# Optimization experiments

Hardware: AMD Instinct MI355X
Metric: run time of the kernel (lower is better)

## Reference

```python
import jax, jax.numpy as jnp
from jax import lax
import numpy as np

NUM_LABELS = 64
ENC_DIM = 256
C = 128            # channels
C2 = 2 * C         # trunk width
OUT_DIM = 512
LAYERS = [(3, 1), (3, 2), (3, 4), (3, 8), (3, 16)]
RF = 1 + sum((k - 1) * d for k, d in LAYERS)   # 63
MAX_T = 48
PAD, START, STOP = 0, 5, 6
BATCH, T_ENC = 8, 64


def setup_inputs() -> dict:
    key = jax.random.key(0)
    ks = jax.random.split(key, 20)

    def w(k, shape, fan_in):
        return (jax.random.normal(k, shape, jnp.float32) * np.sqrt(2.0 / fan_in)).astype(jnp.float32)

    def b(k, shape):
        return 1e-4 * jax.random.normal(k, shape, jnp.float32)

    L = len(LAYERS)
    return {
        'encoded_seq': jax.random.normal(ks[0], (BATCH, ENC_DIM, T_ENC), jnp.float32),
        'embed':  w(ks[1], (NUM_LABELS, C2), NUM_LABELS),
        'w_in':   w(ks[2], (C2, C2), C2),      'b_in':  b(ks[3], (C2,)),
        'w_enc':  w(ks[4], (ENC_DIM, C2), ENC_DIM), 'b_enc': b(ks[5], (C2,)),
        'res_w1': w(ks[6], (L, C2, C), C2),    'res_b1': b(ks[7], (L, C)),
        'res_wd': w(ks[8], (L, 3, C, C), 3 * C), 'res_bd': b(ks[9], (L, C)),
        'res_w2': w(ks[10], (L, C, C2), C),    'res_b2': b(ks[11], (L, C2)),
        'w_o1':   w(ks[12], (C2, OUT_DIM), C2), 'b_o1': b(ks[13], (OUT_DIM,)),
        'w_o2':   w(ks[14], (OUT_DIM, NUM_LABELS), OUT_DIM), 'b_o2': b(ks[15], (NUM_LABELS,)),
    }


def _decode(encoded_seq, embed, w_in, b_in, w_enc, b_enc,
            res_w1, res_b1, res_wd, res_bd, res_w2, res_b2,
            w_o1, b_o1, w_o2, b_o2):
    B = encoded_seq.shape[0]
    # left-pad encoding with rf-1 zeros (torch code leaves these uninitialized; zeros used here)
    encoded_pad = jnp.concatenate(
        [jnp.zeros((B, ENC_DIM, RF - 1), encoded_seq.dtype), encoded_seq], axis=2)

    def linear(labels, enc_win):
        # labels: (B, RF) int32; enc_win: (B, ENC_DIM, RF)
        x = embed[labels]                                     # (B, RF, C2)
        x = x @ w_in + b_in                                   # input 1x1 conv
        x = x + jnp.einsum('bct,cd->btd', enc_win, w_enc) + b_enc
        for i, (kk, d) in enumerate(LAYERS):                  # ReLU residual blocks
            h = jax.nn.relu(x)
            h = jax.nn.relu(h @ res_w1[i] + res_b1[i])        # 2c -> c
            h = lax.conv_general_dilated(                     # causal dilated conv c -> c
                h, res_wd[i], window_strides=(1,), padding=[((kk - 1) * d, 0)],
                rhs_dilation=(d,), dimension_numbers=('NWC', 'WIO', 'NWC')) + res_bd[i]
            h = jax.nn.relu(h)
            x = x + (h @ res_w2[i] + res_b2[i])               # c -> 2c, residual
        o = jax.nn.relu(x @ w_o1 + b_o1) @ w_o2 + b_o2        # (B, RF, NUM_LABELS)
        return o[:, -1, :]                                    # last timestep only

    def step(labels, k):
        enc_win = lax.dynamic_slice(encoded_pad, (0, 0, k), (B, ENC_DIM, RF))
        logit = linear(labels, enc_win)                       # (B, NUM_LABELS)
        nxt = jnp.argmax(logit, axis=-1).astype(jnp.int32)
        labels = jnp.concatenate([labels[:, 1:], nxt[:, None]], axis=1)
        return labels, (logit, nxt)

    init_labels = jnp.concatenate(
        [jnp.full((B, RF - 1), PAD, jnp.int32), jnp.full((B, 1), START, jnp.int32)], axis=1)
    _, (logits, nexts) = lax.scan(step, init_labels, jnp.arange(MAX_T))
    logits = jnp.transpose(logits, (1, 2, 0))                 # (B, NUM_LABELS, T)
    stopped = jnp.cumsum((nexts == STOP).astype(jnp.int32), axis=0) >= 1  # (T, B), incl. current step
    lengths = (MAX_T - stopped.sum(axis=0)).astype(jnp.int32)
    return logits, lengths


def reference(encoded_seq, embed, w_in, b_in, w_enc, b_enc,
              res_w1, res_b1, res_wd, res_bd, res_w2, res_b2,
              w_o1, b_o1, w_o2, b_o2):
    return _decode(encoded_seq, embed, w_in, b_in, w_enc, b_enc,
                   res_w1, res_b1, res_wd, res_bd, res_w2, res_b2,
                   w_o1, b_o1, w_o2, b_o2)
```

## Files before the change

### kernel.cpp

```cpp
#include <hip/hip_runtime.h>
#include <hip/hip_bf16.h>

#define NUM_LABELS 64
#define ENC_DIM 256
#define CC 128
#define C2 256
#define OUT_DIM 512
#define NLAYERS 5
#define MAX_T 48
#define BATCH 8
#define T_ENC 64
#define LAB_PAD 0
#define LAB_START 5
#define LAB_STOP 6

__device__ __forceinline__ float dot4(float4 wv, float4 av) {
    return wv.x * av.x + wv.y * av.y + wv.z * av.z + wv.w * av.w;
}

__global__ __launch_bounds__(256) void pre_kernel(
    const float* __restrict__ enc, const float* __restrict__ embed,
    const float* __restrict__ w_in, const float* __restrict__ b_in,
    const float* __restrict__ w_enc, const float* __restrict__ b_enc,
    float* __restrict__ E2, float* __restrict__ encp)
{
    const int t = threadIdx.x;
    const int blk = blockIdx.x;
    if (blk < NUM_LABELS) {
        float acc = b_in[t];
        const float* e = embed + blk * C2;
        for (int j = 0; j < C2; ++j) acc += e[j] * w_in[j * C2 + t];
        E2[blk * C2 + t] = acc;
    } else {
        const int idx = blk - NUM_LABELS;
        const int b = idx / MAX_T;
        const int k = idx % MAX_T;
        float acc = b_enc[t];
        const float* ecol = enc + b * ENC_DIM * T_ENC + k;
        for (int c = 0; c < ENC_DIM; ++c) acc += ecol[c * T_ENC] * w_enc[c * C2 + t];
        encp[idx * C2 + t] = acc;
    }
}

__global__ __launch_bounds__(256) void prefix_kernel(
    const float* __restrict__ embed, const float* __restrict__ w_in,
    const float* __restrict__ b_in,  const float* __restrict__ b_enc,
    const float* __restrict__ w1,    const float* __restrict__ b1,
    const float* __restrict__ wd,    const float* __restrict__ bd,
    const float* __restrict__ w2,    const float* __restrict__ b2,
    float* __restrict__ h0out)
{
    const int t = threadIdx.x;
    __shared__ float x[C2];
    __shared__ float r[C2];
    __shared__ float h[CC];
    __shared__ float hr[CC];

    {
        float acc = b_in[t] + b_enc[t];
        const float* e = embed + LAB_PAD * C2;
        for (int j = 0; j < C2; ++j) acc += e[j] * w_in[j * C2 + t];
        x[t] = acc;
    }
    __syncthreads();

    for (int i = 0; i < NLAYERS; ++i) {
        r[t] = fmaxf(x[t], 0.f);
        __syncthreads();
        if (t < CC) {
            float a = b1[i * CC + t];
            const float* W = w1 + (i * C2) * CC + t;
            for (int j = 0; j < C2; ++j) a += r[j] * W[j * CC];
            float hv = fmaxf(a, 0.f);
            h[t] = hv;
            h0out[i * CC + t] = hv;
        }
        __syncthreads();
        if (t < CC) {
            float a = bd[i * CC + t];
            const float* W0 = wd + ((i * 3 + 0) * CC) * CC + t;
            const float* W1 = wd + ((i * 3 + 1) * CC) * CC + t;
            const float* W2 = wd + ((i * 3 + 2) * CC) * CC + t;
            for (int c = 0; c < CC; ++c)
                a += h[c] * (W0[c * CC] + W1[c * CC] + W2[c * CC]);
            hr[t] = fmaxf(a, 0.f);
        }
        __syncthreads();
        {
            float a = b2[i * C2 + t];
            const float* W = w2 + (i * CC) * C2 + t;
            for (int c = 0; c < CC; ++c) a += hr[c] * W[c * C2];
            x[t] += a;
        }
        __syncthreads();
    }
}

__global__ __launch_bounds__(256) void repack_w1_kernel(
    const float* __restrict__ src, float4* __restrict__ dst)
{
    const int p = blockIdx.x * 256 + threadIdx.x;
    const int i = p >> 13, q = p & 8191;
    const int m = q >> 10, t = q & 1023;
    const int g = t >> 7, c = t & 127;
    const int r0 = g * 32 + m * 4;
    const float* s = src + (i * 256 + r0) * 128 + c;
    float4 v; v.x = s[0]; v.y = s[128]; v.z = s[256]; v.w = s[384];
    dst[p] = v;
}

__global__ __launch_bounds__(256) void repack_wd_kernel(
    const float* __restrict__ src, float4* __restrict__ dst)
{
    const int p = blockIdx.x * 256 + threadIdx.x;
    const int i = p / 12288, q = p % 12288;
    const int u = q >> 10, t = q & 1023;
    const int tap = u % 3, m = u / 3;
    const int g = t >> 7, c = t & 127;
    const int r0 = g * 16 + m * 4;
    const float* s = src + ((i * 3 + tap) * 128 + r0) * 128 + c;
    float4 v; v.x = s[0]; v.y = s[128]; v.z = s[256]; v.w = s[384];
    dst[p] = v;
}

__global__ __launch_bounds__(256) void repack_w2_kernel(
    const float* __restrict__ src, float4* __restrict__ dst)
{
    const int p = blockIdx.x * 256 + threadIdx.x;
    const int i = p >> 13, q = p & 8191;
    const int m = q >> 10, t = q & 1023;
    const int g = t >> 8, c = t & 255;
    const int r0 = g * 32 + m * 4;
    const float* s = src + (i * 128 + r0) * 256 + c;
    float4 v; v.x = s[0]; v.y = s[256]; v.z = s[512]; v.w = s[768];
    dst[p] = v;
}

__global__ __launch_bounds__(256) void repack_wo1_kernel(
    const float* __restrict__ src, float4* __restrict__ dst)
{
    const int p = blockIdx.x * 256 + threadIdx.x;
    const int m = p >> 10, t = p & 1023;
    const int g = t >> 9, c = t & 511;
    const int r0 = g * 128 + m * 4;
    const float* s = src + r0 * 512 + c;
    float4 v; v.x = s[0]; v.y = s[512]; v.z = s[1024]; v.w = s[1536];
    dst[p] = v;
}

__global__ __launch_bounds__(256) void repack_wo2_kernel(
    const float* __restrict__ src, float4* __restrict__ dst)
{
    const int p = blockIdx.x * 256 + threadIdx.x;
    const int m = p >> 10, t = p & 1023;
    const int g = t >> 6, c = t & 63;
    const int r0 = g * 32 + m * 4;
    const float* s = src + r0 * 64 + c;
    float4 v; v.x = s[0]; v.y = s[64]; v.z = s[128]; v.w = s[192];
    dst[p] = v;
}

__global__ __launch_bounds__(1024) void decode_kernel(
    const float4* __restrict__ w1L,  const float* __restrict__ b1,
    const float4* __restrict__ wdL,  const float* __restrict__ bd,
    const float4* __restrict__ w2L,  const float* __restrict__ b2,
    const float4* __restrict__ wo1L, const float* __restrict__ bo1,
    const float4* __restrict__ wo2L, const float* __restrict__ bo2,
    const float* __restrict__ E2, const float* __restrict__ encp,
    const float* __restrict__ h0g, float* __restrict__ out)
{
    const int b = blockIdx.x;
    const int t = threadIdx.x;

    __shared__ alignas(16) float ring0[3 * CC];
    __shared__ alignas(16) float ring1[5 * CC];
    __shared__ alignas(16) float ring2[9 * CC];
    __shared__ alignas(16) float ring3[17 * CC];
    __shared__ alignas(16) float ring4[33 * CC];
    __shared__ alignas(16) float h0s[NLAYERS * CC];
    __shared__ alignas(16) float xs[C2];
    __shared__ alignas(16) float rs[C2];
    __shared__ alignas(16) float hr[CC];
    __shared__ alignas(16) float us[OUT_DIM];
    __shared__ alignas(16) float part[1024];
    __shared__ float b1s[NLAYERS * CC];
    __shared__ float bds[NLAYERS * CC];
    __shared__ float b2s[NLAYERS * C2];
    __shared__ float bo1s[OUT_DIM];
    __shared__ float bo2s[NUM_LABELS];
    __shared__ int s_lab, s_stop;

    float* rings[NLAYERS] = { ring0, ring1, ring2, ring3, ring4 };
    const int rszc[NLAYERS] = { 3, 5, 9, 17, 33 };

    for (int idx = t; idx < NLAYERS * CC; idx += 1024) {
        h0s[idx] = h0g[idx]; b1s[idx] = b1[idx]; bds[idx] = bd[idx];
    }
    for (int idx = t; idx < NLAYERS * C2; idx += 1024) b2s[idx] = b2[idx];
    for (int idx = t; idx < OUT_DIM; idx += 1024) bo1s[idx] = bo1[idx];
    for (int idx = t; idx < NUM_LABELS; idx += 1024) bo2s[idx] = bo2[idx];
    if (t == 0) { s_lab = LAB_START; s_stop = MAX_T; }
    __syncthreads();

    for (int k = 0; k < MAX_T; ++k) {
        if (t < C2) {
            float xv = E2[s_lab * C2 + t] + encp[(b * MAX_T + k) * C2 + t];
            xs[t] = xv;
            rs[t] = fmaxf(xv, 0.f);
        }
        __syncthreads();

#pragma unroll
        for (int i = 0; i < NLAYERS; ++i) {
            const int d = 1 << i;
            const int rsz = rszc[i];
            const int cslot = k % rsz;
            float* rng = rings[i];

            {
                const int g = t >> 7;
                const float4* Wb = w1L + i * 8192 + t;
                const float4* ra = reinterpret_cast<const float4*>(rs) + g * 8;
                float4 wv[8], av[8];
#pragma unroll
                for (int m = 0; m < 8; ++m) wv[m] = Wb[m * 1024];
#pragma unroll
                for (int m = 0; m < 8; ++m) av[m] = ra[m];
                float acc = 0.f;
#pragma unroll
                for (int m = 0; m < 8; ++m) acc += dot4(wv[m], av[m]);
                part[t] = acc;
            }
            __syncthreads();
            if (t < CC) {
                float s = b1s[i * CC + t];
#pragma unroll
                for (int g2 = 0; g2 < 8; ++g2) s += part[g2 * 128 + t];
                rng[cslot * CC + t] = fmaxf(s, 0.f);
            }
            __syncthreads();

            {
                const int g = t >> 7;
                const float* cur = rng + cslot * CC;
                const float* p1 = (k >= d)     ? rng + ((k - d) % rsz) * CC     : h0s + i * CC;
                const float* p0 = (k >= 2 * d) ? rng + ((k - 2 * d) % rsz) * CC : h0s + i * CC;
                const float4* c4  = reinterpret_cast<const float4*>(cur) + g * 4;
                const float4* a14 = reinterpret_cast<const float4*>(p1) + g * 4;
                const float4* a04 = reinterpret_cast<const float4*>(p0) + g * 4;
                const float4* Wb = wdL + i * 12288 + t;
                float4 wv[12], av[12];
#pragma unroll
                for (int m = 0; m < 4; ++m) {
                    wv[m * 3 + 0] = Wb[(m * 3 + 0) * 1024];
                    wv[m * 3 + 1] = Wb[(m * 3 + 1) * 1024];
                    wv[m * 3 + 2] = Wb[(m * 3 + 2) * 1024];
                }
#pragma unroll
                for (int m = 0; m < 4; ++m) {
                    av[m * 3 + 0] = a04[m];
                    av[m * 3 + 1] = a14[m];
                    av[m * 3 + 2] = c4[m];
                }
                float acc = 0.f;
#pragma unroll
                for (int m = 0; m < 12; ++m) acc += dot4(wv[m], av[m]);
                part[t] = acc;
            }
            __syncthreads();
            if (t < CC) {
                float s = bds[i * CC + t];
#pragma unroll
                for (int g2 = 0; g2 < 8; ++g2) s += part[g2 * 128 + t];
                hr[t] = fmaxf(s, 0.f);
            }
            __syncthreads();

            {
                const int g = t >> 8;
                const float4* Wb = w2L + i * 8192 + t;
                const float4* ha = reinterpret_cast<const float4*>(hr) + g * 8;
                float4 wv[8], av[8];
#pragma unroll
                for (int m = 0; m < 8; ++m) wv[m] = Wb[m * 1024];
#pragma unroll
                for (int m = 0; m < 8; ++m) av[m] = ha[m];
                float acc = 0.f;
#pragma unroll
                for (int m = 0; m < 8; ++m) acc += dot4(wv[m], av[m]);
                part[t] = acc;
            }
            __syncthreads();
            if (t < C2) {
                float s = b2s[i * C2 + t];
#pragma unroll
                for (int g2 = 0; g2 < 4; ++g2) s += part[g2 * 256 + t];
                float xv = xs[t] + s;
                xs[t] = xv;
                rs[t] = fmaxf(xv, 0.f);
            }
            __syncthreads();
        }

        {
            const int g = t >> 9;
            const float4* Wb = wo1L + t;
            const float4* xa = reinterpret_cast<const float4*>(xs) + g * 32;
            float acc = 0.f;
#pragma unroll 1
            for (int mb = 0; mb < 4; ++mb) {
                float4 wv[8], av[8];
#pragma unroll
                for (int m = 0; m < 8; ++m) wv[m] = Wb[(mb * 8 + m) * 1024];
#pragma unroll
                for (int m = 0; m < 8; ++m) av[m] = xa[mb * 8 + m];
#pragma unroll
                for (int m = 0; m < 8; ++m) acc += dot4(wv[m], av[m]);
            }
            part[t] = acc;
        }
        __syncthreads();
        if (t < OUT_DIM) us[t] = fmaxf(part[t] + part[t + 512] + bo1s[t], 0.f);
        __syncthreads();

        {
            const int g = t >> 6;
            const float4* Wb = wo2L + t;
            const float4* ua = reinterpret_cast<const float4*>(us) + g * 8;
            float4 wv[8], av[8];
#pragma unroll
            for (int m = 0; m < 8; ++m) wv[m] = Wb[m * 1024];
#pragma unroll
            for (int m = 0; m < 8; ++m) av[m] = ua[m];
            float acc = 0.f;
#pragma unroll
            for (int m = 0; m < 8; ++m) acc += dot4(wv[m], av[m]);
            part[t] = acc;
        }
        __syncthreads();
        if (t < NUM_LABELS) {
            float v = bo2s[t];
#pragma unroll
            for (int g2 = 0; g2 < 16; ++g2) v += part[g2 * 64 + t];
            out[(b * NUM_LABELS + t) * MAX_T + k] = v;
            float bv = v; int bi = t;
#pragma unroll
            for (int off = 32; off; off >>= 1) {
                float ov = __shfl_xor(bv, off);
                int oi = __shfl_xor(bi, off);
                if (ov > bv || (ov == bv && oi < bi)) { bv = ov; bi = oi; }
            }
            if (t == 0) {
                s_lab = bi;
                if (bi == LAB_STOP && s_stop == MAX_T) s_stop = k;
            }
        }
        __syncthreads();
    }

    if (t == 0) out[BATCH * NUM_LABELS * MAX_T + b] = (float)s_stop;
}

extern "C" void kernel_launch(void* const* d_in, const int* in_sizes, int n_in,
                              void* d_out, int out_size, void* d_ws, size_t ws_size,
                              hipStream_t stream) {
    const float* enc   = (const float*)d_in[0];
    const float* embed = (const float*)d_in[1];
    const float* w_in  = (const float*)d_in[2];
    const float* b_in  = (const float*)d_in[3];
    const float* w_enc = (const float*)d_in[4];
    const float* b_enc = (const float*)d_in[5];
    const float* w1    = (const float*)d_in[6];
    const float* b1    = (const float*)d_in[7];
    const float* wd    = (const float*)d_in[8];
    const float* bd    = (const float*)d_in[9];
    const float* w2    = (const float*)d_in[10];
    const float* b2    = (const float*)d_in[11];
    const float* wo1   = (const float*)d_in[12];
    const float* bo1   = (const float*)d_in[13];
    const float* wo2   = (const float*)d_in[14];
    const float* bo2   = (const float*)d_in[15];
    float* out = (float*)d_out;
    float* wsf = (float*)d_ws;

    float* E2   = wsf;
    float* encp = wsf + 16384;
    float* h0   = wsf + 16384 + 98304;
    float4* w1L  = (float4*)(wsf + 115328);
    float4* wdL  = w1L + 40960;
    float4* w2L  = wdL + 61440;
    float4* wo1L = w2L + 40960;
    float4* wo2L = wo1L + 32768;

    pre_kernel<<<NUM_LABELS + BATCH * MAX_T, 256, 0, stream>>>(
        enc, embed, w_in, b_in, w_enc, b_enc, E2, encp);
    prefix_kernel<<<1, 256, 0, stream>>>(
        embed, w_in, b_in, b_enc, w1, b1, wd, bd, w2, b2, h0);
    repack_w1_kernel<<<160, 256, 0, stream>>>(w1, w1L);
    repack_wd_kernel<<<240, 256, 0, stream>>>(wd, wdL);
    repack_w2_kernel<<<160, 256, 0, stream>>>(w2, w2L);
    repack_wo1_kernel<<<128, 256, 0, stream>>>(wo1, wo1L);
    repack_wo2_kernel<<<32, 256, 0, stream>>>(wo2, wo2L);
    decode_kernel<<<BATCH, 1024, 0, stream>>>(
        w1L, b1, wdL, bd, w2L, b2, wo1L, bo1, wo2L, bo2, E2, encp, h0, out);
}
```

Baseline: 3.406 ms.

## Split decode across 8 workgroups per batch with global-atomic inter-block sync

Each batch's sequential decode was handled by a single 1024-thread workgroup that streamed all weights from global or L2 memory every step. It now runs on 8 cooperating 256-thread workgroups per batch, 64 in total. Each workgroup owns an output slice, keeps its weight slice in registers, and prefetches the next layer's weights while waiting. Partial activations are exchanged through global memory using agent-scope atomics and counter-based spin barriers. This adds cross-CU synchronisation latency at every matvec stage in exchange for more parallel compute and less weight traffic per workgroup, and it relies on all 64 blocks being co-resident.

```diff
diff --git a/kernel.cpp b/kernel.cpp
--- a/kernel.cpp
+++ b/kernel.cpp
@@ -14,8 +14,22 @@
 #define LAB_START 5
 #define LAB_STOP 6
 
+#define AGENT __HIP_MEMORY_SCOPE_AGENT
+
 __device__ __forceinline__ float dot4(float4 wv, float4 av) {
     return wv.x * av.x + wv.y * av.y + wv.z * av.z + wv.w * av.w;
+}
+
+__device__ __forceinline__ void sync_signal(int* ctr, int t) {
+    __builtin_amdgcn_fence(__ATOMIC_RELEASE, "agent");
+    if (t == 0) __hip_atomic_fetch_add(ctr, 1, __ATOMIC_RELAXED, AGENT);
+}
+__device__ __forceinline__ void sync_wait(int* ctr, int t, int target) {
+    if (t == 0) {
+        while (__hip_atomic_load(ctr, __ATOMIC_RELAXED, AGENT) < target) {}
+    }
+    __builtin_amdgcn_fence(__ATOMIC_ACQUIRE, "agent");
+    __syncthreads();
 }
 
 __global__ __launch_bounds__(256) void pre_kernel(
@@ -100,77 +114,88 @@
     const float* __restrict__ src, float4* __restrict__ dst)
 {
     const int p = blockIdx.x * 256 + threadIdx.x;
-    const int i = p >> 13, q = p & 8191;
-    const int m = q >> 10, t = q & 1023;
-    const int g = t >> 7, c = t & 127;
-    const int r0 = g * 32 + m * 4;
-    const float* s = src + (i * 256 + r0) * 128 + c;
-    float4 v; v.x = s[0]; v.y = s[128]; v.z = s[256]; v.w = s[384];
-    dst[p] = v;
+    const int si = p >> 10, c = p & 1023;
+    const int s = si / 5, i = si % 5;
+    const int m = c >> 8, tt = c & 255;
+    const int g = tt >> 4, o = tt & 15;
+    const float* b = src + (i * 256 + g * 16 + m * 4) * 128 + s * 16 + o;
+    float4 v; v.x = b[0]; v.y = b[128]; v.z = b[256]; v.w = b[384];
+    dst[s * 23040 + i * 3584 + c] = v;
 }
 
 __global__ __launch_bounds__(256) void repack_wd_kernel(
     const float* __restrict__ src, float4* __restrict__ dst)
 {
     const int p = blockIdx.x * 256 + threadIdx.x;
-    const int i = p / 12288, q = p % 12288;
-    const int u = q >> 10, t = q & 1023;
-    const int tap = u % 3, m = u / 3;
-    const int g = t >> 7, c = t & 127;
-    const int r0 = g * 16 + m * 4;
-    const float* s = src + ((i * 3 + tap) * 128 + r0) * 128 + c;
-    float4 v; v.x = s[0]; v.y = s[128]; v.z = s[256]; v.w = s[384];
-    dst[p] = v;
+    const int si = p / 1536, c = p % 1536;
+    const int s = si / 5, i = si % 5;
+    const int u = c >> 8, tt = c & 255;
+    const int tap = u >> 1, m = u & 1;
+    const int g = tt >> 4, o = tt & 15;
+    const float* b = src + ((i * 3 + tap) * 128 + g * 8 + m * 4) * 128 + s * 16 + o;
+    float4 v; v.x = b[0]; v.y = b[128]; v.z = b[256]; v.w = b[384];
+    dst[s * 23040 + i * 3584 + 1024 + c] = v;
 }
 
 __global__ __launch_bounds__(256) void repack_w2_kernel(
     const float* __restrict__ src, float4* __restrict__ dst)
 {
     const int p = blockIdx.x * 256 + threadIdx.x;
-    const int i = p >> 13, q = p & 8191;
-    const int m = q >> 10, t = q & 1023;
-    const int g = t >> 8, c = t & 255;
-    const int r0 = g * 32 + m * 4;
-    const float* s = src + (i * 128 + r0) * 256 + c;
-    float4 v; v.x = s[0]; v.y = s[256]; v.z = s[512]; v.w = s[768];
-    dst[p] = v;
+    const int si = p >> 10, c = p & 1023;
+    const int s = si / 5, i = si % 5;
+    const int m = c >> 8, tt = c & 255;
+    const int g = tt >> 5, o = tt & 31;
+    const float* b = src + (i * 128 + g * 16 + m * 4) * 256 + s * 32 + o;
+    float4 v; v.x = b[0]; v.y = b[256]; v.z = b[512]; v.w = b[768];
+    dst[s * 23040 + i * 3584 + 2560 + c] = v;
 }
 
 __global__ __launch_bounds__(256) void repack_wo1_kernel(
     const float* __restrict__ src, float4* __restrict__ dst)
 {
     const int p = blockIdx.x * 256 + threadIdx.x;
-    const int m = p >> 10, t = p & 1023;
-    const int g = t >> 9, c = t & 511;
-    const int r0 = g * 128 + m * 4;
-    const float* s = src + r0 * 512 + c;
-    float4 v; v.x = s[0]; v.y = s[512]; v.z = s[1024]; v.w = s[1536];
-    dst[p] = v;
+    const int s = p >> 12, c = p & 4095;
+    const int m = c >> 8, tt = c & 255;
+    const int g = tt >> 6, o = tt & 63;
+    const float* b = src + (g * 64 + m * 4) * 512 + s * 64 + o;
+    float4 v; v.x = b[0]; v.y = b[512]; v.z = b[1024]; v.w = b[1536];
+    dst[s * 23040 + 17920 + c] = v;
 }
 
 __global__ __launch_bounds__(256) void repack_wo2_kernel(
     const float* __restrict__ src, float4* __restrict__ dst)
 {
     const int p = blockIdx.x * 256 + threadIdx.x;
-    const int m = p >> 10, t = p & 1023;
-    const int g = t >> 6, c = t & 63;
-    const int r0 = g * 32 + m * 4;
-    const float* s = src + r0 * 64 + c;
-    float4 v; v.x = s[0]; v.y = s[64]; v.z = s[128]; v.w = s[192];
-    dst[p] = v;
-}
-
-__global__ __launch_bounds__(1024) void decode_kernel(
-    const float4* __restrict__ w1L,  const float* __restrict__ b1,
-    const float4* __restrict__ wdL,  const float* __restrict__ bd,
-    const float4* __restrict__ w2L,  const float* __restrict__ b2,
-    const float4* __restrict__ wo1L, const float* __restrict__ bo1,
-    const float4* __restrict__ wo2L, const float* __restrict__ bo2,
+    const int s = p >> 10, c = p & 1023;
+    const int m = c >> 8, tt = c & 255;
+    const int g = tt >> 3, o = tt & 7;
+    const float* b = src + (g * 16 + m * 4) * 64 + s * 8 + o;
+    float4 v; v.x = b[0]; v.y = b[64]; v.z = b[128]; v.w = b[192];
+    dst[s * 23040 + 22016 + c] = v;
+}
+
+__global__ __launch_bounds__(256) void init_ctr_kernel(int* __restrict__ ctrs)
+{
+    const int idx = blockIdx.x * 256 + threadIdx.x;
+    if (idx < 512) ctrs[idx] = 0;
+}
+
+__global__ __launch_bounds__(256) void decode_kernel(
+    const float4* __restrict__ Wall,
+    const float* __restrict__ b1, const float* __restrict__ bd,
+    const float* __restrict__ b2, const float* __restrict__ bo1,
+    const float* __restrict__ bo2,
     const float* __restrict__ E2, const float* __restrict__ encp,
-    const float* __restrict__ h0g, float* __restrict__ out)
-{
-    const int b = blockIdx.x;
+    const float* __restrict__ h0g,
+    float* __restrict__ actH, float* __restrict__ actHR,
+    float* __restrict__ actX, float* __restrict__ actU,
+    float* __restrict__ actLG, int* __restrict__ ctrs,
+    float* __restrict__ out)
+{
+    const int e = blockIdx.x & 7;
+    const int s = blockIdx.x >> 3;
     const int t = threadIdx.x;
+    const float4* W4 = Wall + s * 23040;
 
     __shared__ alignas(16) float ring0[3 * CC];
     __shared__ alignas(16) float ring1[5 * CC];
@@ -180,31 +205,30 @@
     __shared__ alignas(16) float h0s[NLAYERS * CC];
     __shared__ alignas(16) float xs[C2];
     __shared__ alignas(16) float rs[C2];
-    __shared__ alignas(16) float hr[CC];
+    __shared__ alignas(16) float hfull[CC];
+    __shared__ alignas(16) float hrf[CC];
     __shared__ alignas(16) float us[OUT_DIM];
-    __shared__ alignas(16) float part[1024];
-    __shared__ float b1s[NLAYERS * CC];
-    __shared__ float bds[NLAYERS * CC];
-    __shared__ float b2s[NLAYERS * C2];
-    __shared__ float bo1s[OUT_DIM];
-    __shared__ float bo2s[NUM_LABELS];
+    __shared__ float part[256];
     __shared__ int s_lab, s_stop;
 
-    float* rings[NLAYERS] = { ring0, ring1, ring2, ring3, ring4 };
-    const int rszc[NLAYERS] = { 3, 5, 9, 17, 33 };
-
-    for (int idx = t; idx < NLAYERS * CC; idx += 1024) {
-        h0s[idx] = h0g[idx]; b1s[idx] = b1[idx]; bds[idx] = bd[idx];
-    }
-    for (int idx = t; idx < NLAYERS * C2; idx += 1024) b2s[idx] = b2[idx];
-    for (int idx = t; idx < OUT_DIM; idx += 1024) bo1s[idx] = bo1[idx];
-    for (int idx = t; idx < NUM_LABELS; idx += 1024) bo2s[idx] = bo2[idx];
+    for (int i = t; i < NLAYERS * CC; i += 256) h0s[i] = h0g[i];
     if (t == 0) { s_lab = LAB_START; s_stop = MAX_T; }
     __syncthreads();
 
+    int* ctr = ctrs + e * 64;
+    int target = 8;
+
+    float4 wA[4], wB[6], wC[4], wD[16], wE[4];
+
+    {
+        const float4* p = W4;
+#pragma unroll
+        for (int m = 0; m < 4; ++m) wA[m] = p[m * 256 + t];
+    }
+
     for (int k = 0; k < MAX_T; ++k) {
-        if (t < C2) {
-            float xv = E2[s_lab * C2 + t] + encp[(b * MAX_T + k) * C2 + t];
+        {
+            float xv = E2[s_lab * C2 + t] + encp[(e * MAX_T + k) * C2 + t];
             xs[t] = xv;
             rs[t] = fmaxf(xv, 0.f);
         }
@@ -213,89 +237,108 @@
 #pragma unroll
         for (int i = 0; i < NLAYERS; ++i) {
             const int d = 1 << i;
-            const int rsz = rszc[i];
-            const int cslot = k % rsz;
-            float* rng = rings[i];
-
-            {
-                const int g = t >> 7;
-                const float4* Wb = w1L + i * 8192 + t;
-                const float4* ra = reinterpret_cast<const float4*>(rs) + g * 8;
-                float4 wv[8], av[8];
-#pragma unroll
-                for (int m = 0; m < 8; ++m) wv[m] = Wb[m * 1024];
-#pragma unroll
-                for (int m = 0; m < 8; ++m) av[m] = ra[m];
+            const int rsz = (2 * d + 1);
+            float* rng = (i == 0) ? ring0 : (i == 1) ? ring1 : (i == 2) ? ring2
+                        : (i == 3) ? ring3 : ring4;
+
+            {
+                const int g = t >> 4;
+                const float4* rs4 = (const float4*)rs;
                 float acc = 0.f;
 #pragma unroll
-                for (int m = 0; m < 8; ++m) acc += dot4(wv[m], av[m]);
+                for (int m = 0; m < 4; ++m) acc += dot4(wA[m], rs4[g * 4 + m]);
                 part[t] = acc;
             }
             __syncthreads();
+            if (t < 16) {
+                float v = b1[i * CC + s * 16 + t];
+#pragma unroll
+                for (int j = 0; j < 16; ++j) v += part[t + j * 16];
+                v = fmaxf(v, 0.f);
+                __hip_atomic_store(&actH[e * CC + s * 16 + t], v, __ATOMIC_RELAXED, AGENT);
+            }
+            sync_signal(ctr, t);
+            {
+                const float4* p = W4 + i * 3584 + 1024;
+#pragma unroll
+                for (int u = 0; u < 6; ++u) wB[u] = p[u * 256 + t];
+            }
+            sync_wait(ctr, t, target);
+            target += 8;
             if (t < CC) {
-                float s = b1s[i * CC + t];
-#pragma unroll
-                for (int g2 = 0; g2 < 8; ++g2) s += part[g2 * 128 + t];
-                rng[cslot * CC + t] = fmaxf(s, 0.f);
-            }
-            __syncthreads();
-
-            {
-                const int g = t >> 7;
-                const float* cur = rng + cslot * CC;
+                float hv = __hip_atomic_load(&actH[e * CC + t], __ATOMIC_RELAXED, AGENT);
+                hfull[t] = hv;
+                rng[(k % rsz) * CC + t] = hv;
+            }
+            __syncthreads();
+
+            {
+                const int g = t >> 4;
                 const float* p1 = (k >= d)     ? rng + ((k - d) % rsz) * CC     : h0s + i * CC;
                 const float* p0 = (k >= 2 * d) ? rng + ((k - 2 * d) % rsz) * CC : h0s + i * CC;
-                const float4* c4  = reinterpret_cast<const float4*>(cur) + g * 4;
-                const float4* a14 = reinterpret_cast<const float4*>(p1) + g * 4;
-                const float4* a04 = reinterpret_cast<const float4*>(p0) + g * 4;
-                const float4* Wb = wdL + i * 12288 + t;
-                float4 wv[12], av[12];
-#pragma unroll
-                for (int m = 0; m < 4; ++m) {
-                    wv[m * 3 + 0] = Wb[(m * 3 + 0) * 1024];
-                    wv[m * 3 + 1] = Wb[(m * 3 + 1) * 1024];
-                    wv[m * 3 + 2] = Wb[(m * 3 + 2) * 1024];
+                const float4* a0 = (const float4*)p0;
+                const float4* a1 = (const float4*)p1;
+                const float4* a2 = (const float4*)hfull;
+                float acc = 0.f;
+#pragma unroll
+                for (int m = 0; m < 2; ++m) {
+                    acc += dot4(wB[0 * 2 + m], a0[g * 2 + m]);
+                    acc += dot4(wB[1 * 2 + m], a1[g * 2 + m]);
+                    acc += dot4(wB[2 * 2 + m], a2[g * 2 + m]);
                 }
-#pragma unroll
-                for (int m = 0; m < 4; ++m) {
-                    av[m * 3 + 0] = a04[m];
-                    av[m * 3 + 1] = a14[m];
-                    av[m * 3 + 2] = c4[m];
-                }
+                part[t] = acc;
+            }
+            __syncthreads();
+            if (t < 16) {
+                float v = bd[i * CC + s * 16 + t];
+#pragma unroll
+                for (int j = 0; j < 16; ++j) v += part[t + j * 16];
+                v = fmaxf(v, 0.f);
+                __hip_atomic_store(&actHR[e * CC + s * 16 + t], v, __ATOMIC_RELAXED, AGENT);
+            }
+            sync_signal(ctr, t);
+            {
+                const float4* p = W4 + i * 3584 + 2560;
+#pragma unroll
+                for (int m = 0; m < 4; ++m) wC[m] = p[m * 256 + t];
+            }
+            sync_wait(ctr, t, target);
+            target += 8;
+            if (t < CC) {
+                hrf[t] = __hip_atomic_load(&actHR[e * CC + t], __ATOMIC_RELAXED, AGENT);
+            }
+            __syncthreads();
+
+            {
+                const int g = t >> 5;
+                const float4* h4 = (const float4*)hrf;
                 float acc = 0.f;
 #pragma unroll
-                for (int m = 0; m < 12; ++m) acc += dot4(wv[m], av[m]);
+                for (int m = 0; m < 4; ++m) acc += dot4(wC[m], h4[g * 4 + m]);
                 part[t] = acc;
             }
             __syncthreads();
-            if (t < CC) {
-                float s = bds[i * CC + t];
-#pragma unroll
-                for (int g2 = 0; g2 < 8; ++g2) s += part[g2 * 128 + t];
-                hr[t] = fmaxf(s, 0.f);
-            }
-            __syncthreads();
-
-            {
-                const int g = t >> 8;
-                const float4* Wb = w2L + i * 8192 + t;
-                const float4* ha = reinterpret_cast<const float4*>(hr) + g * 8;
-                float4 wv[8], av[8];
-#pragma unroll
-                for (int m = 0; m < 8; ++m) wv[m] = Wb[m * 1024];
-#pragma unroll
-                for (int m = 0; m < 8; ++m) av[m] = ha[m];
-                float acc = 0.f;
-#pragma unroll
-                for (int m = 0; m < 8; ++m) acc += dot4(wv[m], av[m]);
-                part[t] = acc;
-            }
-            __syncthreads();
-            if (t < C2) {
-                float s = b2s[i * C2 + t];
-#pragma unroll
-                for (int g2 = 0; g2 < 4; ++g2) s += part[g2 * 256 + t];
-                float xv = xs[t] + s;
+            if (t < 32) {
+                float v = b2[i * C2 + s * 32 + t];
+#pragma unroll
+                for (int j = 0; j < 8; ++j) v += part[t + j * 32];
+                __hip_atomic_store(&actX[e * C2 + s * 32 + t], v, __ATOMIC_RELAXED, AGENT);
+            }
+            sync_signal(ctr, t);
+            if (i < 4) {
+                const float4* p = W4 + (i + 1) * 3584;
+#pragma unroll
+                for (int m = 0; m < 4; ++m) wA[m] = p[m * 256 + t];
+            } else {
+                const float4* p = W4 + 17920;
+#pragma unroll
+                for (int m = 0; m < 16; ++m) wD[m] = p[m * 256 + t];
+            }
+            sync_wait(ctr, t, target);
+            target += 8;
+            {
+                float dv = __hip_atomic_load(&actX[e * C2 + t], __ATOMIC_RELAXED, AGENT);
+                float xv = xs[t] + dv;
                 xs[t] = xv;
                 rs[t] = fmaxf(xv, 0.f);
             }
@@ -303,46 +346,59 @@
         }
 
         {
-            const int g = t >> 9;
-            const float4* Wb = wo1L + t;
-            const float4* xa = reinterpret_cast<const float4*>(xs) + g * 32;
+            const int g = t >> 6;
+            const float4* x4 = (const float4*)xs;
             float acc = 0.f;
-#pragma unroll 1
-            for (int mb = 0; mb < 4; ++mb) {
-                float4 wv[8], av[8];
-#pragma unroll
-                for (int m = 0; m < 8; ++m) wv[m] = Wb[(mb * 8 + m) * 1024];
-#pragma unroll
-                for (int m = 0; m < 8; ++m) av[m] = xa[mb * 8 + m];
-#pragma unroll
-                for (int m = 0; m < 8; ++m) acc += dot4(wv[m], av[m]);
-            }
+#pragma unroll
+            for (int m = 0; m < 16; ++m) acc += dot4(wD[m], x4[g * 16 + m]);
             part[t] = acc;
         }
         __syncthreads();
-        if (t < OUT_DIM) us[t] = fmaxf(part[t] + part[t + 512] + bo1s[t], 0.f);
-        __syncthreads();
-
-        {
-            const int g = t >> 6;
-            const float4* Wb = wo2L + t;
-            const float4* ua = reinterpret_cast<const float4*>(us) + g * 8;
-            float4 wv[8], av[8];
-#pragma unroll
-            for (int m = 0; m < 8; ++m) wv[m] = Wb[m * 1024];
-#pragma unroll
-            for (int m = 0; m < 8; ++m) av[m] = ua[m];
+        if (t < 64) {
+            float v = bo1[s * 64 + t];
+#pragma unroll
+            for (int j = 0; j < 4; ++j) v += part[t + j * 64];
+            v = fmaxf(v, 0.f);
+            __hip_atomic_store(&actU[e * OUT_DIM + s * 64 + t], v, __ATOMIC_RELAXED, AGENT);
+        }
+        sync_signal(ctr, t);
+        {
+            const float4* p = W4 + 22016;
+#pragma unroll
+            for (int m = 0; m < 4; ++m) wE[m] = p[m * 256 + t];
+        }
+        sync_wait(ctr, t, target);
+        target += 8;
+        for (int idx = t; idx < OUT_DIM; idx += 256)
+            us[idx] = __hip_atomic_load(&actU[e * OUT_DIM + idx], __ATOMIC_RELAXED, AGENT);
+        __syncthreads();
+
+        {
+            const int g = t >> 3;
+            const float4* u4 = (const float4*)us;
             float acc = 0.f;
 #pragma unroll
-            for (int m = 0; m < 8; ++m) acc += dot4(wv[m], av[m]);
+            for (int m = 0; m < 4; ++m) acc += dot4(wE[m], u4[g * 4 + m]);
             part[t] = acc;
         }
         __syncthreads();
+        if (t < 8) {
+            float v = bo2[s * 8 + t];
+#pragma unroll
+            for (int j = 0; j < 32; ++j) v += part[t + j * 8];
+            __hip_atomic_store(&actLG[e * NUM_LABELS + s * 8 + t], v, __ATOMIC_RELAXED, AGENT);
+        }
+        sync_signal(ctr, t);
+        {
+            const float4* p = W4;
+#pragma unroll
+            for (int m = 0; m < 4; ++m) wA[m] = p[m * 256 + t];
+        }
+        sync_wait(ctr, t, target);
+        target += 8;
         if (t < NUM_LABELS) {
-            float v = bo2s[t];
-#pragma unroll
-            for (int g2 = 0; g2 < 16; ++g2) v += part[g2 * 64 + t];
-            out[(b * NUM_LABELS + t) * MAX_T + k] = v;
+            float v = __hip_atomic_load(&actLG[e * NUM_LABELS + t], __ATOMIC_RELAXED, AGENT);
+            if (s == 0) out[(e * NUM_LABELS + t) * MAX_T + k] = v;
             float bv = v; int bi = t;
 #pragma unroll
             for (int off = 32; off; off >>= 1) {
@@ -358,7 +414,7 @@
         __syncthreads();
     }
 
-    if (t == 0) out[BATCH * NUM_LABELS * MAX_T + b] = (float)s_stop;
+    if (s == 0 && t == 0) out[BATCH * NUM_LABELS * MAX_T + e] = (float)s_stop;
 }
 
 extern "C" void kernel_launch(void* const* d_in, const int* in_sizes, int n_in,
@@ -386,21 +442,26 @@
     float* E2   = wsf;
     float* encp = wsf + 16384;
     float* h0   = wsf + 16384 + 98304;
-    float4* w1L  = (float4*)(wsf + 115328);
-    float4* wdL  = w1L + 40960;
-    float4* w2L  = wdL + 61440;
-    float4* wo1L = w2L + 40960;
-    float4* wo2L = wo1L + 32768;
+    float4* Wall = (float4*)(wsf + 115328);
+    float* acts  = wsf + 115328 + 737280;
+    float* actH  = acts;
+    float* actHR = actH + 1024;
+    float* actX  = actHR + 1024;
+    float* actU  = actX + 2048;
+    float* actLG = actU + 4096;
+    int*   ctrs  = (int*)(actLG + 512);
 
     pre_kernel<<<NUM_LABELS + BATCH * MAX_T, 256, 0, stream>>>(
         enc, embed, w_in, b_in, w_enc, b_enc, E2, encp);
     prefix_kernel<<<1, 256, 0, stream>>>(
         embed, w_in, b_in, b_enc, w1, b1, wd, bd, w2, b2, h0);
-    repack_w1_kernel<<<160, 256, 0, stream>>>(w1, w1L);
-    repack_wd_kernel<<<240, 256, 0, stream>>>(wd, wdL);
-    repack_w2_kernel<<<160, 256, 0, stream>>>(w2, w2L);
-    repack_wo1_kernel<<<128, 256, 0, stream>>>(wo1, wo1L);
-    repack_wo2_kernel<<<32, 256, 0, stream>>>(wo2, wo2L);
-    decode_kernel<<<BATCH, 1024, 0, stream>>>(
-        w1L, b1, wdL, bd, w2L, b2, wo1L, bo1, wo2L, bo2, E2, encp, h0, out);
-}
+    repack_w1_kernel<<<160, 256, 0, stream>>>(w1, Wall);
+    repack_wd_kernel<<<240, 256, 0, stream>>>(wd, Wall);
+    repack_w2_kernel<<<160, 256, 0, stream>>>(w2, Wall);
+    repack_wo1_kernel<<<128, 256, 0, stream>>>(wo1, Wall);
+    repack_wo2_kernel<<<32, 256, 0, stream>>>(wo2, Wall);
+    init_ctr_kernel<<<2, 256, 0, stream>>>(ctrs);
+    decode_kernel<<<64, 256, 0, stream>>>(
+        Wall, b1, bd, b2, bo1, bo2, E2, encp, h0,
+        actH, actHR, actX, actU, actLG, ctrs, out);
+}
```

New measurement: 3.867 ms. 1.14x slower.
